# Kernel tuning notes

Hardware: AMD Instinct MI355X
Metric: run time of the kernel (lower is better)

The kernel has to match this reference:

```python
import jax, jax.numpy as jnp
import numpy as np

E = 1024      # emb_dim
H = 16        # num_heads
DH = E // H   # per-head atten_dim
B = 2
T = 2048


def _layernorm(x, scale, shift, eps=1e-5):
    mean = x.mean(axis=-1, keepdims=True)
    var = ((x - mean) ** 2).mean(axis=-1, keepdims=True)  # unbiased=False
    return scale * (x - mean) / jnp.sqrt(var + eps) + shift


def _gelu(x):
    # Faithful to source: tanh(sqrt(2/pi)*x + 0.044715*x^3)  (no sqrt on cubic term)
    c = jnp.sqrt(jnp.asarray(2.0 / jnp.pi, x.dtype))
    return 0.5 * x * (1.0 + jnp.tanh(c * x + 0.044715 * x ** 3))


def setup_inputs() -> dict:
    key = jax.random.key(0)
    ks = jax.random.split(key, 12)
    s = 0.02
    return {
        "x":     jax.random.normal(ks[0], (B, T, E), jnp.float32),
        "Wq":    jax.random.normal(ks[1], (H, E, DH), jnp.float32) * s,
        "Wk":    jax.random.normal(ks[2], (H, E, DH), jnp.float32) * s,
        "Wv":    jax.random.normal(ks[3], (H, E, DH), jnp.float32) * s,
        "fc_w":  jax.random.normal(ks[4], (E, E), jnp.float32) * s,
        "fc_b":  jnp.zeros((E,), jnp.float32),
        "ln1_s": jnp.ones((E,), jnp.float32),
        "ln1_b": jnp.zeros((E,), jnp.float32),
        "ln2_s": jnp.ones((E,), jnp.float32),
        "ln2_b": jnp.zeros((E,), jnp.float32),
        "ff_w1": jax.random.normal(ks[5], (E, 4 * E), jnp.float32) * s,
        "ff_b1": jnp.zeros((4 * E,), jnp.float32),
        "ff_w2": jax.random.normal(ks[6], (4 * E, E), jnp.float32) * s,
        "ff_b2": jnp.zeros((E,), jnp.float32),
    }


def _attention(x, Wq, Wk, Wv, fc_w, fc_b):
    b, t, _ = x.shape
    q = jnp.einsum("bte,hed->bhtd", x, Wq)
    k = jnp.einsum("bte,hed->bhtd", x, Wk)
    v = jnp.einsum("bte,hed->bhtd", x, Wv)
    scores = jnp.einsum("bhtd,bhsd->bhts", q, k)
    causal = jnp.triu(jnp.ones((t, t), bool), 1)
    scores = jnp.where(causal, -jnp.inf, scores)
    w = jax.nn.softmax(scores / jnp.sqrt(jnp.asarray(DH, x.dtype)), axis=-1)
    ctx = jnp.einsum("bhts,bhsd->bhtd", w, v)
    # faithful quirk from source: per-head transpose(1,2) then reshape(b, T, d_out)
    ctx = jnp.swapaxes(ctx, 2, 3).reshape(b, H, t, DH)
    concat = ctx.transpose(0, 2, 1, 3).reshape(b, t, E)
    return concat @ fc_w + fc_b


def reference(x, Wq, Wk, Wv, fc_w, fc_b, ln1_s, ln1_b, ln2_s, ln2_b,
              ff_w1, ff_b1, ff_w2, ff_b2):
    h = _attention(_layernorm(x, ln1_s, ln1_b), Wq, Wk, Wv, fc_w, fc_b) + x
    y = _layernorm(h, ln2_s, ln2_b)
    y = _gelu(y @ ff_w1 + ff_b1) @ ff_w2 + ff_b2
    return y + h
```

## Files before the change

kernel.cpp:

```cpp
#include <hip/hip_runtime.h>


#define En 1024
#define Hn 16
#define DHn 64
#define Bn 2
#define Tn 2048
#define Mrows 4096

typedef __attribute__((ext_vector_type(8))) short bf16x8;
typedef __attribute__((ext_vector_type(4))) float f32x4;

__device__ __forceinline__ short f2bf(float f) {
    unsigned u = __float_as_uint(f);
    u += 0x7FFFu + ((u >> 16) & 1u);
    return (short)(u >> 16);
}
__device__ __forceinline__ ushort f2bfu(float f) {
    unsigned u = __float_as_uint(f);
    u += 0x7FFFu + ((u >> 16) & 1u);
    return (ushort)(u >> 16);
}
__device__ __forceinline__ float bf2f(ushort u) {
    return __uint_as_float((unsigned)u << 16);
}

__device__ __forceinline__ float gelu_f(float x) {
    float u = 0.79788456080286535588f * x + 0.044715f * x * x * x;
    float t = __expf(2.0f * u);
    return x * t / (t + 1.0f);
}

__device__ __forceinline__ void load_lds16(const void* g, void* l) {
    __builtin_amdgcn_global_load_lds(
        (const __attribute__((address_space(1))) unsigned int*)(uintptr_t)g,
        (__attribute__((address_space(3))) unsigned int*)(uintptr_t)l,
        16, 0, 0);
}

__global__ __launch_bounds__(256) void ln_kernel(
    const float* __restrict__ in, const float* __restrict__ sc,
    const float* __restrict__ sh, ushort* __restrict__ out)
{
    int row = blockIdx.x;
    int tid = threadIdx.x;
    float4 v = ((const float4*)(in + (size_t)row * En))[tid];
    float s  = v.x + v.y + v.z + v.w;
    float s2 = v.x*v.x + v.y*v.y + v.z*v.z + v.w*v.w;
    #pragma unroll
    for (int off = 32; off > 0; off >>= 1) {
        s  += __shfl_down(s,  off);
        s2 += __shfl_down(s2, off);
    }
    __shared__ float red[2][4];
    int wave = tid >> 6, lane = tid & 63;
    if (lane == 0) { red[0][wave] = s; red[1][wave] = s2; }
    __syncthreads();
    s  = red[0][0] + red[0][1] + red[0][2] + red[0][3];
    s2 = red[1][0] + red[1][1] + red[1][2] + red[1][3];
    float mean = s * (1.0f / En);
    float var  = s2 * (1.0f / En) - mean * mean;
    float r = rsqrtf(var + 1e-5f);
    float4 scv = ((const float4*)sc)[tid];
    float4 shv = ((const float4*)sh)[tid];
    ushort4 o;
    o.x = f2bfu(scv.x * (v.x - mean) * r + shv.x);
    o.y = f2bfu(scv.y * (v.y - mean) * r + shv.y);
    o.z = f2bfu(scv.z * (v.z - mean) * r + shv.z);
    o.w = f2bfu(scv.w * (v.w - mean) * r + shv.w);
    ((ushort4*)(out + (size_t)row * En))[tid] = o;
}

__global__ __launch_bounds__(256) void ln2_fuse(
    const float* __restrict__ P0, const float* __restrict__ P1,
    const float* __restrict__ bias, const float* __restrict__ x,
    const float* __restrict__ sc, const float* __restrict__ sh,
    ushort* __restrict__ hb, ushort* __restrict__ ynb)
{
    int row = blockIdx.x, tid = threadIdx.x;
    size_t idx = (size_t)row * 256 + tid;
    float4 a  = ((const float4*)P0)[idx];
    float4 b  = ((const float4*)P1)[idx];
    float4 bi = ((const float4*)bias)[tid];
    float4 xr = ((const float4*)x)[idx];
    float4 v;
    v.x = a.x + b.x + bi.x + xr.x;
    v.y = a.y + b.y + bi.y + xr.y;
    v.z = a.z + b.z + bi.z + xr.z;
    v.w = a.w + b.w + bi.w + xr.w;
    ushort4 hv;
    hv.x = f2bfu(v.x); hv.y = f2bfu(v.y); hv.z = f2bfu(v.z); hv.w = f2bfu(v.w);
    ((ushort4*)hb)[idx] = hv;
    float s  = v.x + v.y + v.z + v.w;
    float s2 = v.x*v.x + v.y*v.y + v.z*v.z + v.w*v.w;
    #pragma unroll
    for (int off = 32; off > 0; off >>= 1) {
        s  += __shfl_down(s,  off);
        s2 += __shfl_down(s2, off);
    }
    __shared__ float red[2][4];
    int wave = tid >> 6, lane = tid & 63;
    if (lane == 0) { red[0][wave] = s; red[1][wave] = s2; }
    __syncthreads();
    s  = red[0][0] + red[0][1] + red[0][2] + red[0][3];
    s2 = red[1][0] + red[1][1] + red[1][2] + red[1][3];
    float mean = s * (1.0f / En);
    float var  = s2 * (1.0f / En) - mean * mean;
    float r = rsqrtf(var + 1e-5f);
    float4 scv = ((const float4*)sc)[tid];
    float4 shv = ((const float4*)sh)[tid];
    ushort4 o;
    o.x = f2bfu(scv.x * (v.x - mean) * r + shv.x);
    o.y = f2bfu(scv.y * (v.y - mean) * r + shv.y);
    o.z = f2bfu(scv.z * (v.z - mean) * r + shv.z);
    o.w = f2bfu(scv.w * (v.w - mean) * r + shv.w);
    ((ushort4*)ynb)[idx] = o;
}

__global__ __launch_bounds__(256) void ff2_reduce(
    const float* __restrict__ P0, const float* __restrict__ P1,
    const float* __restrict__ bias, const ushort* __restrict__ hb,
    float* __restrict__ out)
{
    int tid = threadIdx.x;
    size_t i = (size_t)blockIdx.x * 256 + tid;
    float4 a  = ((const float4*)P0)[i];
    float4 b  = ((const float4*)P1)[i];
    float4 bi = ((const float4*)bias)[tid];
    ushort4 hu = ((const ushort4*)hb)[i];
    float4 o;
    o.x = a.x + b.x + bi.x + bf2f(hu.x);
    o.y = a.y + b.y + bi.y + bf2f(hu.y);
    o.z = a.z + b.z + bi.z + bf2f(hu.z);
    o.w = a.w + b.w + bi.w + bf2f(hu.w);
    ((float4*)out)[i] = o;
}

__global__ __launch_bounds__(256) void transpose_w(
    const float* __restrict__ in, ushort* __restrict__ out, int K, int N)
{
    __shared__ float t[64][65];
    int k0 = blockIdx.x * 64, n0 = blockIdx.y * 64;
    int tid = threadIdx.x, r = tid >> 4, c4 = (tid & 15) * 4;
    #pragma unroll
    for (int i = 0; i < 4; ++i) {
        float4 v = *(const float4*)(in + (size_t)(k0 + r + i * 16) * N + n0 + c4);
        t[r + i * 16][c4 + 0] = v.x; t[r + i * 16][c4 + 1] = v.y;
        t[r + i * 16][c4 + 2] = v.z; t[r + i * 16][c4 + 3] = v.w;
    }
    __syncthreads();
    #pragma unroll
    for (int i = 0; i < 4; ++i) {
        int n = r + i * 16;
        ushort4 u;
        u.x = f2bfu(t[c4 + 0][n]); u.y = f2bfu(t[c4 + 1][n]);
        u.z = f2bfu(t[c4 + 2][n]); u.w = f2bfu(t[c4 + 3][n]);
        *(ushort4*)(out + (size_t)(n0 + n) * K + k0 + c4) = u;
    }
}

__global__ __launch_bounds__(256) void transpose_qkv(
    const float* __restrict__ Wq, const float* __restrict__ Wk,
    const float* __restrict__ Wv, ushort* __restrict__ out)
{
    __shared__ float t[64][65];
    int z = blockIdx.z, sel = z >> 4, h = z & 15;
    const float* in = (sel == 0 ? Wq : sel == 1 ? Wk : Wv) + (size_t)h * En * DHn;
    ushort* o = out + ((size_t)(sel * 1024 + h * 64)) * En;
    int k0 = blockIdx.x * 64;
    int tid = threadIdx.x, r = tid >> 4, c4 = (tid & 15) * 4;
    #pragma unroll
    for (int i = 0; i < 4; ++i) {
        float4 v = *(const float4*)(in + (size_t)(k0 + r + i * 16) * DHn + c4);
        t[r + i * 16][c4 + 0] = v.x; t[r + i * 16][c4 + 1] = v.y;
        t[r + i * 16][c4 + 2] = v.z; t[r + i * 16][c4 + 3] = v.w;
    }
    __syncthreads();
    #pragma unroll
    for (int i = 0; i < 4; ++i) {
        int n = r + i * 16;
        ushort4 u;
        u.x = f2bfu(t[c4 + 0][n]); u.y = f2bfu(t[c4 + 1][n]);
        u.z = f2bfu(t[c4 + 2][n]); u.w = f2bfu(t[c4 + 3][n]);
        *(ushort4*)(o + (size_t)n * En + k0 + c4) = u;
    }
}

template<int MODE, int TN>
__global__ __launch_bounds__(256) void gemm_bf16(
    const ushort* __restrict__ A, int lda,
    const ushort* __restrict__ Bt, int ldb, int Kloop,
    const float* __restrict__ bias,
    float* __restrict__ Cf, ushort* __restrict__ Cb, int ldc,
    ushort* __restrict__ qo, ushort* __restrict__ ko, ushort* __restrict__ vo)
{
    constexpr int WCN = TN / 2;
    constexpr int NI  = WCN / 16;
    constexpr int BIW = TN * 8 / 256;
    constexpr int STAGE = 128 * 64 + TN * 64;
    constexpr int SMEMN = (MODE == 2 && STAGE < 4 * 64 * 68) ? 4 * 64 * 68 : STAGE;
    __shared__ ushort smem[SMEMN];
    ushort* As = smem;
    ushort* Bs = smem + 128 * 64;
    int tid = threadIdx.x, wv = tid >> 6, lid = tid & 63;
    int m0 = blockIdx.x * 128, n0 = blockIdx.y * TN;
    int koff = blockIdx.z * Kloop;
    int wr = wv >> 1, wc = wv & 1;
    int hm = lid & 15, hk = lid >> 4;

    f32x4 acc[4][NI];
    #pragma unroll
    for (int i = 0; i < 4; ++i)
        #pragma unroll
        for (int j = 0; j < NI; ++j) acc[i][j] = (f32x4){0.f, 0.f, 0.f, 0.f};

    const ushort* Abase = A + (size_t)m0 * lda + koff;
    const ushort* Bbase = Bt + (size_t)n0 * ldb + koff;

    for (int k0 = 0; k0 < Kloop; k0 += 64) {
        __syncthreads();
        #pragma unroll
        for (int i = 0; i < 4; ++i) {
            int c = wv * 256 + i * 64 + lid;
            int r = c >> 3, s = c & 7;
            int j = s ^ (r & 7);
            load_lds16(Abase + (size_t)r * lda + k0 + j * 8,
                       &As[(wv * 256 + i * 64) * 8]);
        }
        #pragma unroll
        for (int i = 0; i < BIW; ++i) {
            int c = wv * (BIW * 64) + i * 64 + lid;
            int r = c >> 3, s = c & 7;
            int j = s ^ (r & 7);
            load_lds16(Bbase + (size_t)r * ldb + k0 + j * 8,
                       &Bs[(wv * (BIW * 64) + i * 64) * 8]);
        }
        __syncthreads();
        #pragma unroll
        for (int kk = 0; kk < 2; ++kk) {
            bf16x8 af[4], bfr[NI];
            #pragma unroll
            for (int mi = 0; mi < 4; ++mi) {
                int r = wr * 64 + mi * 16 + hm;
                int slot = ((kk << 2) | hk) ^ (r & 7);
                af[mi] = *(const bf16x8*)&As[(r * 8 + slot) * 8];
            }
            #pragma unroll
            for (int ni = 0; ni < NI; ++ni) {
                int r = wc * WCN + ni * 16 + hm;
                int slot = ((kk << 2) | hk) ^ (r & 7);
                bfr[ni] = *(const bf16x8*)&Bs[(r * 8 + slot) * 8];
            }
            #pragma unroll
            for (int mi = 0; mi < 4; ++mi)
                #pragma unroll
                for (int ni = 0; ni < NI; ++ni)
                    acc[mi][ni] = __builtin_amdgcn_mfma_f32_16x16x32_bf16(
                        af[mi], bfr[ni], acc[mi][ni], 0, 0, 0);
        }
    }

    int colbase = n0 + wc * WCN + hm;
    int rowbase = m0 + wr * 64 + hk * 4;
    if (MODE == 1) {
        #pragma unroll
        for (int ni = 0; ni < NI; ++ni) {
            int col = colbase + ni * 16;
            float bb = bias[col];
            #pragma unroll
            for (int mi = 0; mi < 4; ++mi) {
                int row = rowbase + mi * 16;
                #pragma unroll
                for (int r = 0; r < 4; ++r)
                    Cb[(size_t)(row + r) * ldc + col] =
                        f2bfu(gelu_f(acc[mi][ni][r] + bb));
            }
        }
    } else if (MODE == 2) {
        __syncthreads();
        ushort* Ls = smem + wv * (64 * 68);
        int col0 = n0 + wc * 64;
        int sel = col0 >> 10, h = (col0 & 1023) >> 6;
        if (sel < 2) {
            #pragma unroll
            for (int ni = 0; ni < NI; ++ni)
                #pragma unroll
                for (int mi = 0; mi < 4; ++mi)
                    #pragma unroll
                    for (int r = 0; r < 4; ++r)
                        Ls[(mi * 16 + hk * 4 + r) * 68 + ni * 16 + hm] =
                            f2bfu(acc[mi][ni][r]);
            ushort* outp = (sel == 0 ? qo : ko) + (size_t)h * (Mrows * DHn);
            int dcol = hm * 4;
            #pragma unroll
            for (int i = 0; i < 16; ++i) {
                int t = hk + i * 4;
                *(ushort4*)(outp + (size_t)(m0 + wr * 64 + t) * DHn + dcol) =
                    *(const ushort4*)&Ls[t * 68 + dcol];
            }
        } else {
            #pragma unroll
            for (int ni = 0; ni < NI; ++ni)
                #pragma unroll
                for (int mi = 0; mi < 4; ++mi)
                    #pragma unroll
                    for (int r = 0; r < 4; ++r)
                        Ls[(ni * 16 + hm) * 68 + mi * 16 + hk * 4 + r] =
                            f2bfu(acc[mi][ni][r]);
            int bb2 = m0 >> 11;
            int t0 = (m0 & 2047) + wr * 64;
            ushort* outp = vo + ((size_t)((h * 2 + bb2) * 64)) * Tn + t0;
            int tcol = hm * 4;
            #pragma unroll
            for (int i = 0; i < 16; ++i) {
                int d = hk + i * 4;
                *(ushort4*)(outp + (size_t)d * Tn + tcol) =
                    *(const ushort4*)&Ls[d * 68 + tcol];
            }
        }
    } else {
        float* Cp = Cf + (size_t)blockIdx.z * Mrows * ldc;
        #pragma unroll
        for (int ni = 0; ni < NI; ++ni) {
            int col = colbase + ni * 16;
            #pragma unroll
            for (int mi = 0; mi < 4; ++mi) {
                int row = rowbase + mi * 16;
                #pragma unroll
                for (int r = 0; r < 4; ++r)
                    Cp[(size_t)(row + r) * ldc + col] = acc[mi][ni][r];
            }
        }
    }
}

__global__ __launch_bounds__(256) void attn_mfma(
    const ushort* __restrict__ q, const ushort* __restrict__ ksrc,
    const ushort* __restrict__ vtsrc, ushort* __restrict__ cat)
{
    int g = blockIdx.x;
    int h = g >> 1, b = g & 1;
    const ushort* qg  = q     + (size_t)g * Tn * DHn;
    const ushort* kg  = ksrc  + (size_t)g * Tn * DHn;
    const ushort* vtg = vtsrc + (size_t)g * DHn * Tn;
    int tid = threadIdx.x, wave = tid >> 6, lane = tid & 63;
    int m = lane & 15, gq = lane >> 4;

    __shared__ short Ks[4096];
    __shared__ short Vt[4096];
    __shared__ short Ps[4][1024];

    int R  = tid >> 2;
    int c2 = tid & 3;

    #pragma unroll 1
    for (int phase = 0; phase < 2; ++phase) {
        int qt = phase ? (31 - (int)blockIdx.y) : (int)blockIdx.y;
        int q0 = qt * 64;

        bf16x8 qf[2];
        {
            const ushort* qp = qg + (size_t)(q0 + wave * 16 + m) * DHn + gq * 8;
            qf[0] = *(const bf16x8*)(qp);
            qf[1] = *(const bf16x8*)(qp + 32);
        }
        f32x4 o[4];
        #pragma unroll
        for (int i = 0; i < 4; ++i) o[i] = (f32x4){0.f, 0.f, 0.f, 0.f};
        float lsum[4] = {0.f, 0.f, 0.f, 0.f};

        for (int kt = 0; kt <= qt; ++kt) {
            int k0 = kt * 64;
            __syncthreads();
            {
                const ushort* ksp = kg  + (size_t)(k0 + R) * DHn + c2 * 16;
                const ushort* vsp = vtg + (size_t)R * Tn + k0 + c2 * 16;
                bf16x8 f0 = *(const bf16x8*)(ksp);
                bf16x8 f1 = *(const bf16x8*)(ksp + 8);
                bf16x8 v0 = *(const bf16x8*)(vsp);
                bf16x8 v1 = *(const bf16x8*)(vsp + 8);
                *(bf16x8*)&Ks[R * 64 + (((c2 * 2    ) ^ (R & 7)) << 3)] = f0;
                *(bf16x8*)&Ks[R * 64 + (((c2 * 2 + 1) ^ (R & 7)) << 3)] = f1;
                *(bf16x8*)&Vt[R * 64 + (((c2 * 2    ) ^ (R & 7)) << 3)] = v0;
                *(bf16x8*)&Vt[R * 64 + (((c2 * 2 + 1) ^ (R & 7)) << 3)] = v1;
            }
            __syncthreads();

            bool diag = (kt == qt);
            float ps[4][4];
            #pragma unroll
            for (int ct = 0; ct < 4; ++ct) {
                if (diag && ct > wave) {
                    ps[ct][0] = ps[ct][1] = ps[ct][2] = ps[ct][3] = 0.f;
                    continue;
                }
                f32x4 acc = (f32x4){0.f, 0.f, 0.f, 0.f};
                int row = ct * 16 + m;
                #pragma unroll
                for (int db = 0; db < 2; ++db) {
                    bf16x8 kf = *(const bf16x8*)&Ks[row * 64 + (((db * 4 + gq) ^ (row & 7)) << 3)];
                    acc = __builtin_amdgcn_mfma_f32_16x16x32_bf16(qf[db], kf, acc, 0, 0, 0);
                }
                #pragma unroll
                for (int r = 0; r < 4; ++r) {
                    float p;
                    if (diag && (ct * 16 + m) > (wave * 16 + gq * 4 + r)) {
                        p = 0.f;
                    } else {
                        p = __expf(acc[r] * 0.125f);
                    }
                    ps[ct][r] = p;
                    lsum[r] += p;
                }
            }

            #pragma unroll
            for (int ct = 0; ct < 4; ++ct)
                #pragma unroll
                for (int r = 0; r < 4; ++r) {
                    int row = gq * 4 + r;
                    Ps[wave][row * 64 + ((((ct * 2 + (m >> 3)) ^ (row & 7)) << 3) | (m & 7))] =
                        f2bf(ps[ct][r]);
                }
            bf16x8 pf[2];
            #pragma unroll
            for (int db2 = 0; db2 < 2; ++db2)
                pf[db2] = *(const bf16x8*)&Ps[wave][m * 64 + (((db2 * 4 + gq) ^ (m & 7)) << 3)];

            #pragma unroll
            for (int ct2 = 0; ct2 < 4; ++ct2) {
                int row = ct2 * 16 + m;
                #pragma unroll
                for (int db2 = 0; db2 < 2; ++db2) {
                    bf16x8 vf = *(const bf16x8*)&Vt[row * 64 + (((db2 * 4 + gq) ^ (row & 7)) << 3)];
                    o[ct2] = __builtin_amdgcn_mfma_f32_16x16x32_bf16(pf[db2], vf, o[ct2], 0, 0, 0);
                }
            }
        }

        float inv[4];
        #pragma unroll
        for (int r = 0; r < 4; ++r) {
            float l = lsum[r];
            l += __shfl_xor(l, 1);
            l += __shfl_xor(l, 2);
            l += __shfl_xor(l, 4);
            l += __shfl_xor(l, 8);
            inv[r] = 1.0f / l;
        }
        size_t base = (size_t)b * Tn * En + (size_t)h * 64 + (size_t)qt * En
                    + wave * 16 + gq * 4;
        #pragma unroll
        for (int ct2 = 0; ct2 < 4; ++ct2) {
            int d = ct2 * 16 + m;
            #pragma unroll
            for (int r = 0; r < 4; ++r)
                cat[base + (size_t)d * 32 * En + r] = f2bfu(o[ct2][r] * inv[r]);
        }
    }
}

extern "C" void kernel_launch(void* const* d_in, const int* in_sizes, int n_in,
                              void* d_out, int out_size, void* d_ws, size_t ws_size,
                              hipStream_t stream) {
    const float* x     = (const float*)d_in[0];
    const float* Wq    = (const float*)d_in[1];
    const float* Wk    = (const float*)d_in[2];
    const float* Wv    = (const float*)d_in[3];
    const float* fc_w  = (const float*)d_in[4];
    const float* fc_b  = (const float*)d_in[5];
    const float* ln1_s = (const float*)d_in[6];
    const float* ln1_b = (const float*)d_in[7];
    const float* ln2_s = (const float*)d_in[8];
    const float* ln2_b = (const float*)d_in[9];
    const float* ff_w1 = (const float*)d_in[10];
    const float* ff_b1 = (const float*)d_in[11];
    const float* ff_w2 = (const float*)d_in[12];
    const float* ff_b2 = (const float*)d_in[13];
    float* out = (float*)d_out;
    (void)in_sizes; (void)n_in; (void)out_size; (void)ws_size;

    const size_t MB = 1048576;
    char* w8 = (char*)d_ws;
    ushort* S0   = (ushort*)(w8 + 0 * MB);
    ushort* kb   = (ushort*)(w8 + 8 * MB);
    ushort* vtb  = (ushort*)(w8 + 16 * MB);
    ushort* qb   = (ushort*)(w8 + 24 * MB);
    ushort* hb   = (ushort*)(w8 + 32 * MB);
    ushort* y1   = (ushort*)(w8 + 48 * MB);
    float*  Pfc  = (float*)(w8 + 48 * MB);
    float*  Pff2 = (float*)(w8 + 0 * MB);
    ushort* wqkv = (ushort*)(w8 + 80 * MB);
    ushort* wfc  = (ushort*)(w8 + 86 * MB);
    ushort* wf1  = (ushort*)(w8 + 88 * MB);
    ushort* wf2  = (ushort*)(w8 + 96 * MB);

    transpose_qkv<<<dim3(16, 1, 48), 256, 0, stream>>>(Wq, Wk, Wv, wqkv);
    transpose_w<<<dim3(16, 16), 256, 0, stream>>>(fc_w, wfc, En, En);
    transpose_w<<<dim3(16, 64), 256, 0, stream>>>(ff_w1, wf1, En, 4 * En);
    transpose_w<<<dim3(64, 16), 256, 0, stream>>>(ff_w2, wf2, 4 * En, En);

    ln_kernel<<<dim3(Mrows), 256, 0, stream>>>(x, ln1_s, ln1_b, S0);
    gemm_bf16<2, 128><<<dim3(32, 24), 256, 0, stream>>>(
        S0, En, wqkv, En, En, nullptr, nullptr, nullptr, 0, qb, kb, vtb);
    attn_mfma<<<dim3(Hn * Bn, 16), 256, 0, stream>>>(qb, kb, vtb, S0);
    gemm_bf16<3, 64><<<dim3(32, 16, 2), 256, 0, stream>>>(
        S0, En, wfc, En, En / 2, nullptr, Pfc, nullptr, En, nullptr, nullptr, nullptr);
    ln2_fuse<<<dim3(Mrows), 256, 0, stream>>>(
        Pfc, Pfc + (size_t)Mrows * En, fc_b, x, ln2_s, ln2_b, hb, qb);
    gemm_bf16<1, 128><<<dim3(32, 32), 256, 0, stream>>>(
        qb, En, wf1, En, En, ff_b1, nullptr, y1, 4 * En, nullptr, nullptr, nullptr);
    gemm_bf16<3, 64><<<dim3(32, 16, 2), 256, 0, stream>>>(
        y1, 4 * En, wf2, 4 * En, 2 * En, nullptr, Pff2, nullptr, En, nullptr, nullptr, nullptr);
    ff2_reduce<<<dim3(Mrows), 256, 0, stream>>>(
        Pff2, Pff2 + (size_t)Mrows * En, ff_b2, hb, out);
}
```

Measured before the change: 353.5 us.

## Store split-K partials as bf16 via LDS bounce and merge weight transposes

The split-K GEMM partial outputs for the fc and ff2 projections are now written as bf16 through a shared-memory staging tile, using coalesced ushort4 stores instead of scattered fp32 scalar stores. The reducer kernels read bf16 partials and convert them. The four weight-transpose launches are merged into a single prep_w kernel to cut launch overhead. The change halves partial-buffer traffic and makes the stores coalesced, but it rounds each split-K partial to bf16, which loses accuracy.

```diff
diff --git a/kernel.cpp b/kernel.cpp
--- a/kernel.cpp
+++ b/kernel.cpp
@@ -72,22 +72,22 @@
 }
 
 __global__ __launch_bounds__(256) void ln2_fuse(
-    const float* __restrict__ P0, const float* __restrict__ P1,
+    const ushort* __restrict__ P0, const ushort* __restrict__ P1,
     const float* __restrict__ bias, const float* __restrict__ x,
     const float* __restrict__ sc, const float* __restrict__ sh,
     ushort* __restrict__ hb, ushort* __restrict__ ynb)
 {
     int row = blockIdx.x, tid = threadIdx.x;
     size_t idx = (size_t)row * 256 + tid;
-    float4 a  = ((const float4*)P0)[idx];
-    float4 b  = ((const float4*)P1)[idx];
+    ushort4 a = ((const ushort4*)P0)[idx];
+    ushort4 b = ((const ushort4*)P1)[idx];
     float4 bi = ((const float4*)bias)[tid];
     float4 xr = ((const float4*)x)[idx];
     float4 v;
-    v.x = a.x + b.x + bi.x + xr.x;
-    v.y = a.y + b.y + bi.y + xr.y;
-    v.z = a.z + b.z + bi.z + xr.z;
-    v.w = a.w + b.w + bi.w + xr.w;
+    v.x = bf2f(a.x) + bf2f(b.x) + bi.x + xr.x;
+    v.y = bf2f(a.y) + bf2f(b.y) + bi.y + xr.y;
+    v.z = bf2f(a.z) + bf2f(b.z) + bi.z + xr.z;
+    v.w = bf2f(a.w) + bf2f(b.w) + bi.w + xr.w;
     ushort4 hv;
     hv.x = f2bfu(v.x); hv.y = f2bfu(v.y); hv.z = f2bfu(v.z); hv.w = f2bfu(v.w);
     ((ushort4*)hb)[idx] = hv;
@@ -118,29 +118,53 @@
 }
 
 __global__ __launch_bounds__(256) void ff2_reduce(
-    const float* __restrict__ P0, const float* __restrict__ P1,
+    const ushort* __restrict__ P0, const ushort* __restrict__ P1,
     const float* __restrict__ bias, const ushort* __restrict__ hb,
     float* __restrict__ out)
 {
     int tid = threadIdx.x;
     size_t i = (size_t)blockIdx.x * 256 + tid;
-    float4 a  = ((const float4*)P0)[i];
-    float4 b  = ((const float4*)P1)[i];
+    ushort4 a = ((const ushort4*)P0)[i];
+    ushort4 b = ((const ushort4*)P1)[i];
     float4 bi = ((const float4*)bias)[tid];
     ushort4 hu = ((const ushort4*)hb)[i];
     float4 o;
-    o.x = a.x + b.x + bi.x + bf2f(hu.x);
-    o.y = a.y + b.y + bi.y + bf2f(hu.y);
-    o.z = a.z + b.z + bi.z + bf2f(hu.z);
-    o.w = a.w + b.w + bi.w + bf2f(hu.w);
+    o.x = bf2f(a.x) + bf2f(b.x) + bi.x + bf2f(hu.x);
+    o.y = bf2f(a.y) + bf2f(b.y) + bi.y + bf2f(hu.y);
+    o.z = bf2f(a.z) + bf2f(b.z) + bi.z + bf2f(hu.z);
+    o.w = bf2f(a.w) + bf2f(b.w) + bi.w + bf2f(hu.w);
     ((float4*)out)[i] = o;
 }
 
-__global__ __launch_bounds__(256) void transpose_w(
-    const float* __restrict__ in, ushort* __restrict__ out, int K, int N)
+__global__ __launch_bounds__(256) void prep_w(
+    const float* __restrict__ Wq, const float* __restrict__ Wk,
+    const float* __restrict__ Wv, const float* __restrict__ fc_w,
+    const float* __restrict__ ff_w1, const float* __restrict__ ff_w2,
+    ushort* __restrict__ wqkv, ushort* __restrict__ wfc,
+    ushort* __restrict__ wf1, ushort* __restrict__ wf2)
 {
+    int bid = blockIdx.x;
+    const float* in; ushort* out; int N, ldo, k0, n0;
+    if (bid < 768) {
+        int z = bid >> 4, kb = bid & 15;
+        int sel = z / 16, h = z % 16;
+        in  = (sel == 0 ? Wq : sel == 1 ? Wk : Wv) + (size_t)h * En * DHn;
+        out = wqkv + (size_t)(sel * 1024 + h * 64) * En;
+        N = DHn; ldo = En; k0 = kb * 64; n0 = 0;
+    } else if (bid < 1024) {
+        int b2 = bid - 768;
+        in = fc_w; out = wfc; N = En; ldo = En;
+        k0 = (b2 & 15) * 64; n0 = (b2 >> 4) * 64;
+    } else if (bid < 2048) {
+        int b2 = bid - 1024;
+        in = ff_w1; out = wf1; N = 4 * En; ldo = En;
+        k0 = (b2 & 15) * 64; n0 = (b2 >> 4) * 64;
+    } else {
+        int b2 = bid - 2048;
+        in = ff_w2; out = wf2; N = En; ldo = 4 * En;
+        k0 = (b2 & 63) * 64; n0 = (b2 >> 6) * 64;
+    }
     __shared__ float t[64][65];
-    int k0 = blockIdx.x * 64, n0 = blockIdx.y * 64;
     int tid = threadIdx.x, r = tid >> 4, c4 = (tid & 15) * 4;
     #pragma unroll
     for (int i = 0; i < 4; ++i) {
@@ -155,34 +179,7 @@
         ushort4 u;
         u.x = f2bfu(t[c4 + 0][n]); u.y = f2bfu(t[c4 + 1][n]);
         u.z = f2bfu(t[c4 + 2][n]); u.w = f2bfu(t[c4 + 3][n]);
-        *(ushort4*)(out + (size_t)(n0 + n) * K + k0 + c4) = u;
-    }
-}
-
-__global__ __launch_bounds__(256) void transpose_qkv(
-    const float* __restrict__ Wq, const float* __restrict__ Wk,
-    const float* __restrict__ Wv, ushort* __restrict__ out)
-{
-    __shared__ float t[64][65];
-    int z = blockIdx.z, sel = z >> 4, h = z & 15;
-    const float* in = (sel == 0 ? Wq : sel == 1 ? Wk : Wv) + (size_t)h * En * DHn;
-    ushort* o = out + ((size_t)(sel * 1024 + h * 64)) * En;
-    int k0 = blockIdx.x * 64;
-    int tid = threadIdx.x, r = tid >> 4, c4 = (tid & 15) * 4;
-    #pragma unroll
-    for (int i = 0; i < 4; ++i) {
-        float4 v = *(const float4*)(in + (size_t)(k0 + r + i * 16) * DHn + c4);
-        t[r + i * 16][c4 + 0] = v.x; t[r + i * 16][c4 + 1] = v.y;
-        t[r + i * 16][c4 + 2] = v.z; t[r + i * 16][c4 + 3] = v.w;
-    }
-    __syncthreads();
-    #pragma unroll
-    for (int i = 0; i < 4; ++i) {
-        int n = r + i * 16;
-        ushort4 u;
-        u.x = f2bfu(t[c4 + 0][n]); u.y = f2bfu(t[c4 + 1][n]);
-        u.z = f2bfu(t[c4 + 2][n]); u.w = f2bfu(t[c4 + 3][n]);
-        *(ushort4*)(o + (size_t)n * En + k0 + c4) = u;
+        *(ushort4*)(out + (size_t)(n0 + n) * ldo + k0 + c4) = u;
     }
 }
 
@@ -191,14 +188,15 @@
     const ushort* __restrict__ A, int lda,
     const ushort* __restrict__ Bt, int ldb, int Kloop,
     const float* __restrict__ bias,
-    float* __restrict__ Cf, ushort* __restrict__ Cb, int ldc,
+    ushort* __restrict__ Cb, int ldc,
     ushort* __restrict__ qo, ushort* __restrict__ ko, ushort* __restrict__ vo)
 {
     constexpr int WCN = TN / 2;
     constexpr int NI  = WCN / 16;
     constexpr int BIW = TN * 8 / 256;
     constexpr int STAGE = 128 * 64 + TN * 64;
-    constexpr int SMEMN = (MODE == 2 && STAGE < 4 * 64 * 68) ? 4 * 64 * 68 : STAGE;
+    constexpr int BOUNCE = (MODE == 2) ? 4 * 64 * 68 : (MODE == 3 ? 128 * 68 : 0);
+    constexpr int SMEMN = STAGE > BOUNCE ? STAGE : BOUNCE;
     __shared__ ushort smem[SMEMN];
     ushort* As = smem;
     ushort* Bs = smem + 128 * 64;
@@ -319,17 +317,24 @@
             }
         }
     } else {
-        float* Cp = Cf + (size_t)blockIdx.z * Mrows * ldc;
-        #pragma unroll
-        for (int ni = 0; ni < NI; ++ni) {
-            int col = colbase + ni * 16;
-            #pragma unroll
-            for (int mi = 0; mi < 4; ++mi) {
-                int row = rowbase + mi * 16;
+        __syncthreads();
+        ushort* Ls = smem;
+        #pragma unroll
+        for (int ni = 0; ni < NI; ++ni)
+            #pragma unroll
+            for (int mi = 0; mi < 4; ++mi)
                 #pragma unroll
                 for (int r = 0; r < 4; ++r)
-                    Cp[(size_t)(row + r) * ldc + col] = acc[mi][ni][r];
-            }
+                    Ls[(wr * 64 + mi * 16 + hk * 4 + r) * 68
+                       + wc * WCN + ni * 16 + hm] = f2bfu(acc[mi][ni][r]);
+        __syncthreads();
+        ushort* Cp = Cb + (size_t)blockIdx.z * Mrows * ldc;
+        #pragma unroll
+        for (int it = 0; it < 8; ++it) {
+            int i = it * 1024 + tid * 4;
+            int row = i >> 6, col = i & 63;
+            *(ushort4*)(Cp + (size_t)(m0 + row) * ldc + n0 + col) =
+                *(const ushort4*)&Ls[row * 68 + col];
         }
     }
 }
@@ -487,31 +492,29 @@
     ushort* vtb  = (ushort*)(w8 + 16 * MB);
     ushort* qb   = (ushort*)(w8 + 24 * MB);
     ushort* hb   = (ushort*)(w8 + 32 * MB);
+    ushort* Pfc  = (ushort*)(w8 + 48 * MB);
     ushort* y1   = (ushort*)(w8 + 48 * MB);
-    float*  Pfc  = (float*)(w8 + 48 * MB);
-    float*  Pff2 = (float*)(w8 + 0 * MB);
+    ushort* Pff2 = (ushort*)(w8 + 0 * MB);
     ushort* wqkv = (ushort*)(w8 + 80 * MB);
     ushort* wfc  = (ushort*)(w8 + 86 * MB);
     ushort* wf1  = (ushort*)(w8 + 88 * MB);
     ushort* wf2  = (ushort*)(w8 + 96 * MB);
 
-    transpose_qkv<<<dim3(16, 1, 48), 256, 0, stream>>>(Wq, Wk, Wv, wqkv);
-    transpose_w<<<dim3(16, 16), 256, 0, stream>>>(fc_w, wfc, En, En);
-    transpose_w<<<dim3(16, 64), 256, 0, stream>>>(ff_w1, wf1, En, 4 * En);
-    transpose_w<<<dim3(64, 16), 256, 0, stream>>>(ff_w2, wf2, 4 * En, En);
+    prep_w<<<dim3(3072), 256, 0, stream>>>(
+        Wq, Wk, Wv, fc_w, ff_w1, ff_w2, wqkv, wfc, wf1, wf2);
 
     ln_kernel<<<dim3(Mrows), 256, 0, stream>>>(x, ln1_s, ln1_b, S0);
     gemm_bf16<2, 128><<<dim3(32, 24), 256, 0, stream>>>(
-        S0, En, wqkv, En, En, nullptr, nullptr, nullptr, 0, qb, kb, vtb);
+        S0, En, wqkv, En, En, nullptr, nullptr, 0, qb, kb, vtb);
     attn_mfma<<<dim3(Hn * Bn, 16), 256, 0, stream>>>(qb, kb, vtb, S0);
     gemm_bf16<3, 64><<<dim3(32, 16, 2), 256, 0, stream>>>(
-        S0, En, wfc, En, En / 2, nullptr, Pfc, nullptr, En, nullptr, nullptr, nullptr);
+        S0, En, wfc, En, En / 2, nullptr, Pfc, En, nullptr, nullptr, nullptr);
     ln2_fuse<<<dim3(Mrows), 256, 0, stream>>>(
         Pfc, Pfc + (size_t)Mrows * En, fc_b, x, ln2_s, ln2_b, hb, qb);
     gemm_bf16<1, 128><<<dim3(32, 32), 256, 0, stream>>>(
-        qb, En, wf1, En, En, ff_b1, nullptr, y1, 4 * En, nullptr, nullptr, nullptr);
+        qb, En, wf1, En, En, ff_b1, y1, 4 * En, nullptr, nullptr, nullptr);
     gemm_bf16<3, 64><<<dim3(32, 16, 2), 256, 0, stream>>>(
-        y1, 4 * En, wf2, 4 * En, 2 * En, nullptr, Pff2, nullptr, En, nullptr, nullptr, nullptr);
+        y1, 4 * En, wf2, 4 * En, 2 * En, nullptr, Pff2, En, nullptr, nullptr, nullptr);
     ff2_reduce<<<dim3(Mrows), 256, 0, stream>>>(
         Pff2, Pff2 + (size_t)Mrows * En, ff_b2, hb, out);
 }
```

Result: no change. 353.0 us (-0.2%).
